# Optimization experiments

Hardware: AMD Instinct MI355X
Metric: run time of the kernel (lower is better)

The kernel has to match this reference:

```python
import jax, jax.numpy as jnp
import numpy as np

H = 4      # num_attention_heads
DK = 75    # d_k = hidden_size // H
HID = 300  # hidden_size


def setup_inputs() -> dict:
    key = jax.random.key(0)
    ks = jax.random.split(key, 9)
    B, S = 8, 2048
    query = jax.random.normal(ks[0], (B, S, HID), dtype=jnp.float32)
    key_t = jax.random.normal(ks[1], (B, S, HID), dtype=jnp.float32)
    value = jax.random.normal(ks[2], (B, S, HID), dtype=jnp.float32)
    mask = jax.random.randint(ks[3], (B, S), 0, 2, dtype=jnp.int32)
    scale = 1.0 / np.sqrt(HID)
    Wq = jax.random.normal(ks[4], (HID, HID), dtype=jnp.float32) * scale
    Wk = jax.random.normal(ks[5], (HID, HID), dtype=jnp.float32) * scale
    Wv = jax.random.normal(ks[6], (HID, HID), dtype=jnp.float32) * scale
    Wo = jax.random.normal(ks[7], (HID, HID), dtype=jnp.float32) * scale
    bo = jax.random.normal(ks[8], (HID,), dtype=jnp.float32) * 0.01
    return {"query": query, "key": key_t, "value": value, "mask": mask,
            "Wq": Wq, "Wk": Wk, "Wv": Wv, "Wo": Wo, "bo": bo}


def reference(query, key, value, mask, Wq, Wk, Wv, Wo, bo):
    B, S, _ = query.shape
    # QKV projections (nn.Linear: x @ W.T), split into heads: [B,H,S,DK]
    def proj(x, W):
        return (x @ W.T).reshape(B, S, H, DK).transpose(0, 2, 1, 3)
    q, k, v = proj(query, Wq), proj(key, Wk), proj(value, Wv)
    # scores: [B,H,S,S]
    scores = jnp.einsum('bhqd,bhkd->bhqk', q, k) / jnp.sqrt(jnp.float32(DK))
    # mask outer product 'bi,bj->bij' broadcast over heads; fill zeros with -1e9
    m2 = (mask[:, :, None] * mask[:, None, :])[:, None, :, :]  # [B,1,S,S]
    scores = jnp.where(m2 == 0, jnp.float32(-1e9), scores)
    p_attn = jax.nn.softmax(scores, axis=-1)  # dropout p=0.0 (eval mode)
    x = jnp.einsum('bhqk,bhkd->bhqd', p_attn, v)  # [B,H,S,DK]
    x = x.transpose(0, 2, 1, 3).reshape(B, S, H * DK)
    return x @ Wo.T + bo
```

## Files before the change

### kernel.cpp

```cpp
#include <hip/hip_runtime.h>
#include <math.h>

typedef __bf16 bf16x8 __attribute__((ext_vector_type(8)));
typedef float f32x4 __attribute__((ext_vector_type(4)));
typedef float f32x16 __attribute__((ext_vector_type(16)));
typedef unsigned short u16;
typedef u16 u16x8 __attribute__((ext_vector_type(8)));

#define HID 300
#define NH 4
#define DK 75
#define DKP 80
#define BB 8
#define SS 2048
#define BSROWS (BB*SS)
#define C2   0.16658807f

#define MFMA(a,b,c)   __builtin_amdgcn_mfma_f32_16x16x32_bf16(a,b,c,0,0,0)
#define MFMA32(a,b,c) __builtin_amdgcn_mfma_f32_32x32x16_bf16(a,b,c,0,0,0)

static __device__ __forceinline__ float bf2f(u16 h) {
    return __uint_as_float(((unsigned)h) << 16);
}
static __device__ __forceinline__ void split2(float x, u16& hb, u16& lb) {
    const unsigned u = __float_as_uint(x);
    hb = (u16)(u >> 16);
    const float r = x - __uint_as_float(u & 0xffff0000u);
    lb = (u16)(__float_as_uint(r) >> 16);
}
static __device__ __forceinline__ void split2rne(float x, u16& hb, u16& lb) {
    const unsigned u = __float_as_uint(x);
    const unsigned uh = ((u + 0x7fffu + ((u >> 16) & 1u)) >> 16) << 16;
    hb = (u16)(uh >> 16);
    const float r = x - __uint_as_float(uh);
    lb = (u16)(__float_as_uint(r) >> 16);
}

__global__ __launch_bounds__(256)
void prep_w3(const float* __restrict__ Wq, const float* __restrict__ Wk,
             const float* __restrict__ Wv,
             u16* __restrict__ wph, u16* __restrict__ wpl)
{
    const int idx = blockIdx.x * 256 + threadIdx.x;
    if (idx >= 38400) return;
    const int c8 = idx % 40;
    int r = idx / 40;
    const int n = r % 80; r /= 80;
    const int h = r & 3;  r >>= 2;
    const int mat = r;
    const float* W = (mat == 0) ? Wq : (mat == 1) ? Wk : Wv;
    const int col0 = c8 * 8;
    float v[8];
#pragma unroll
    for (int j = 0; j < 8; ++j) v[j] = 0.f;
    if (n < DK) {
        const float* s = W + (size_t)(h * DK + n) * HID + col0;
        if (col0 + 8 <= HID) {
#pragma unroll
            for (int j = 0; j < 8; ++j) v[j] = s[j];
        } else {
#pragma unroll
            for (int j = 0; j < 8; ++j) v[j] = (col0 + j < HID) ? s[j] : 0.f;
        }
    }
    u16x8 hv, lv;
#pragma unroll
    for (int j = 0; j < 8; ++j) {
        u16 hb, lb;
        split2(v[j], hb, lb);
        hv[j] = hb; lv[j] = lb;
    }
    const size_t base = ((size_t)((mat * 4 + h) * 80 + n)) * 320 + col0;
    *(u16x8*)(wph + base) = hv;
    *(u16x8*)(wpl + base) = lv;
}

static __device__ __forceinline__ void gemm_body(
    char* smem, const float* __restrict__ A, const float* __restrict__ W,
    const u16* __restrict__ Wph, const u16* __restrict__ Wpl,
    const float* __restrict__ bias, u16* __restrict__ hiP, u16* __restrict__ loP,
    float* __restrict__ foutP, const int mode, const int bx, const int h)
{
    u16* Ah = (u16*)smem;
    u16* Al = Ah + 128 * 40;
    u16* Wh = Al + 128 * 40;
    u16* Wl = Wh + 80 * 40;

    const int t = threadIdx.x;
    const int wv = t >> 6, l = t & 63, qc = l & 15, g = l >> 4;
    const int row0 = bx * 128;
    const int b = row0 >> 11;
    const int s0 = row0 & 2047;

    const f32x4 zf = {0.f, 0.f, 0.f, 0.f};
    f32x4 acc[2][5];
#pragma unroll
    for (int mt = 0; mt < 2; ++mt)
#pragma unroll
        for (int nt = 0; nt < 5; ++nt) acc[mt][nt] = zf;

    const int rA = t >> 1, halfA = t & 1;
    float4 aPf[4];
    u16x8 wPfH[2], wPfL[2];
    float4 wPf2[3];

    auto loadA = [&](int step) {
        const int k0 = step * 32 + halfA * 16;
        const float* src = A + (size_t)(row0 + rA) * HID + k0;
#pragma unroll
        for (int c4 = 0; c4 < 4; ++c4) {
            const int k = k0 + c4 * 4;
            float4 v;
            if (k + 4 <= HID) v = *(const float4*)(src + c4 * 4);
            else {
                v.x = (k + 0 < HID) ? src[c4 * 4 + 0] : 0.f;
                v.y = (k + 1 < HID) ? src[c4 * 4 + 1] : 0.f;
                v.z = (k + 2 < HID) ? src[c4 * 4 + 2] : 0.f;
                v.w = (k + 3 < HID) ? src[c4 * 4 + 3] : 0.f;
            }
            aPf[c4] = v;
        }
    };
    auto loadW = [&](int step) {
        const int k0 = step * 32;
        if (mode <= 1) {
#pragma unroll
            for (int j = 0; j < 2; ++j) {
                const int idx = j * 256 + t;
                if (idx < 320) {
                    const int n = idx >> 2, c = idx & 3;
                    const size_t wo = (size_t)(h * 80 + n) * 320 + k0 + c * 8;
                    wPfH[j] = *(const u16x8*)(Wph + wo);
                    wPfL[j] = *(const u16x8*)(Wpl + wo);
                }
            }
        } else {
#pragma unroll
            for (int j = 0; j < 3; ++j) {
                const int idx = j * 256 + t;
                if (idx < 640) {
                    const int n = idx >> 3, c = idx & 7;
                    const int k = k0 + c * 4;
                    float4 v = make_float4(0.f, 0.f, 0.f, 0.f);
                    if (n < DK) {
                        const float* src = W + (size_t)(h * DK + n) * HID + k;
                        if (k + 4 <= HID) v = *(const float4*)src;
                        else {
                            v.x = (k + 0 < HID) ? src[0] : 0.f;
                            v.y = (k + 1 < HID) ? src[1] : 0.f;
                            v.z = (k + 2 < HID) ? src[2] : 0.f;
                            v.w = (k + 3 < HID) ? src[3] : 0.f;
                        }
                    }
                    wPf2[j] = v;
                }
            }
        }
    };
    auto writeA = [&]() {
        u16* dh = Ah + rA * 40 + halfA * 16;
        u16* dl = Al + rA * 40 + halfA * 16;
#pragma unroll
        for (int c4 = 0; c4 < 4; ++c4) {
            ushort4 h4, l4;
            split2(aPf[c4].x, h4.x, l4.x);
            split2(aPf[c4].y, h4.y, l4.y);
            split2(aPf[c4].z, h4.z, l4.z);
            split2(aPf[c4].w, h4.w, l4.w);
            *(ushort4*)(dh + c4 * 4) = h4;
            *(ushort4*)(dl + c4 * 4) = l4;
        }
    };
    auto writeW = [&]() {
        if (mode <= 1) {
#pragma unroll
            for (int j = 0; j < 2; ++j) {
                const int idx = j * 256 + t;
                if (idx < 320) {
                    const int n = idx >> 2, c = idx & 3;
                    *(u16x8*)(Wh + n * 40 + c * 8) = wPfH[j];
                    *(u16x8*)(Wl + n * 40 + c * 8) = wPfL[j];
                }
            }
        } else {
#pragma unroll
            for (int j = 0; j < 3; ++j) {
                const int idx = j * 256 + t;
                if (idx < 640) {
                    const int n = idx >> 3, c = idx & 7;
                    ushort4 h4, l4;
                    split2(wPf2[j].x, h4.x, l4.x);
                    split2(wPf2[j].y, h4.y, l4.y);
                    split2(wPf2[j].z, h4.z, l4.z);
                    split2(wPf2[j].w, h4.w, l4.w);
                    *(ushort4*)(Wh + n * 40 + c * 4) = h4;
                    *(ushort4*)(Wl + n * 40 + c * 4) = l4;
                }
            }
        }
    };

    loadA(0);
    loadW(0);

    for (int step = 0; step < 10; ++step) {
        __syncthreads();
        writeA();
        writeW();
        __syncthreads();
        if (step < 9) {
            loadA(step + 1);
            loadW(step + 1);
        }
        bf16x8 ah[2], al2[2];
#pragma unroll
        for (int mt = 0; mt < 2; ++mt) {
            const int roff = (wv * 32 + mt * 16 + qc) * 40 + g * 8;
            ah[mt]  = *(const bf16x8*)(Ah + roff);
            al2[mt] = *(const bf16x8*)(Al + roff);
        }
#pragma unroll
        for (int nt = 0; nt < 5; ++nt) {
            const int woff = (nt * 16 + qc) * 40 + g * 8;
            const bf16x8 bh = *(const bf16x8*)(Wh + woff);
            const bf16x8 bl = *(const bf16x8*)(Wl + woff);
#pragma unroll
            for (int mt = 0; mt < 2; ++mt) {
                acc[mt][nt] = MFMA(ah[mt],  bh, acc[mt][nt]);
                acc[mt][nt] = MFMA(al2[mt], bh, acc[mt][nt]);
                acc[mt][nt] = MFMA(ah[mt],  bl, acc[mt][nt]);
            }
        }
    }
    __syncthreads();

    if (mode <= 1) {
        unsigned* epi = (unsigned*)smem;
#pragma unroll
        for (int mt = 0; mt < 2; ++mt)
#pragma unroll
            for (int nt = 0; nt < 5; ++nt)
#pragma unroll
                for (int r = 0; r < 4; ++r) {
                    u16 hb, lb;
                    split2rne(acc[mt][nt][r], hb, lb);
                    epi[(wv * 32 + mt * 16 + g * 4 + r) * 84 + nt * 16 + qc] =
                        (unsigned)hb | ((unsigned)lb << 16);
                }
        __syncthreads();
        if (mode == 0) {
            const int r = t >> 1, half = t & 1;
            const unsigned* row = epi + r * 84 + half * 40;
            const size_t base = ((size_t)(b * NH + h) * SS + s0 + r) * DKP + half * 40;
            u16* dh = hiP + base;
#pragma unroll
            for (int i = 0; i < 5; ++i) {
                u16x8 hv, lv;
#pragma unroll
                for (int j = 0; j < 8; ++j) {
                    const unsigned u = row[i * 8 + j];
                    hv[j] = (u16)u; lv[j] = (u16)(u >> 16);
                }
                *(u16x8*)(dh + i * 8) = hv;
                if (loP) *(u16x8*)(loP + base + i * 8) = lv;
            }
        } else {
#pragma unroll
            for (int i = 0; i < 3; ++i) {
                const int idx = i * 256 + t;
                if (idx < 640) {
                    const int d = idx >> 3, sc = (idx & 7) * 16;
                    const size_t base = ((size_t)(b * NH + h) * DKP + d) * SS + s0 + sc;
                    u16* dh = hiP + base;
                    u16x8 h0, h1, l0, l1;
#pragma unroll
                    for (int j = 0; j < 8; ++j) {
                        unsigned u = epi[(sc + j) * 84 + d];
                        h0[j] = (u16)u; l0[j] = (u16)(u >> 16);
                        u = epi[(sc + 8 + j) * 84 + d];
                        h1[j] = (u16)u; l1[j] = (u16)(u >> 16);
                    }
                    *(u16x8*)dh = h0; *(u16x8*)(dh + 8) = h1;
                    if (loP) {
                        *(u16x8*)(loP + base) = l0;
                        *(u16x8*)(loP + base + 8) = l1;
                    }
                }
            }
        }
    } else {
        float* epf = (float*)smem;
#pragma unroll
        for (int mt = 0; mt < 2; ++mt)
#pragma unroll
            for (int nt = 0; nt < 5; ++nt)
#pragma unroll
                for (int r = 0; r < 4; ++r)
                    epf[(wv * 32 + mt * 16 + g * 4 + r) * 84 + nt * 16 + qc] = acc[mt][nt][r];
        __syncthreads();
        for (int i = 0; i < 38; ++i) {
            const int idx = i * 256 + t;
            if (idx < 128 * DK) {
                const int r = idx / DK, c = idx - r * DK;
                foutP[(size_t)(row0 + r) * HID + h * DK + c] = epf[r * 84 + c] + bias[h * DK + c];
            }
        }
    }
}

__global__ __launch_bounds__(256)
void proj3_gemm(const float* __restrict__ Aq, const float* __restrict__ Ak,
                const float* __restrict__ Av,
                const u16* __restrict__ wph, const u16* __restrict__ wpl,
                u16* __restrict__ qh, u16* __restrict__ ql,
                u16* __restrict__ kh, u16* __restrict__ vh)
{
    __shared__ char smem[43008];
    const int z = blockIdx.z;
    const float* A = (z == 0) ? Aq : (z == 1) ? Ak : Av;
    const size_t WMAT = (size_t)4 * 80 * 320;
    u16* hiP = (z == 0) ? qh : (z == 1) ? kh : vh;
    u16* loP = (z == 0) ? ql : nullptr;
    const int mode = (z == 2) ? 1 : 0;
    gemm_body(smem, A, nullptr, wph + z * WMAT, wpl + z * WMAT,
              nullptr, hiP, loP, nullptr, mode, blockIdx.x, blockIdx.y);
}

__global__ __launch_bounds__(256)
void out_gemm(const float* __restrict__ A, const float* __restrict__ W,
              const float* __restrict__ bias, float* __restrict__ out)
{
    __shared__ char smem[43008];
    gemm_body(smem, A, W, nullptr, nullptr, bias, nullptr, nullptr, out, 2,
              blockIdx.x, blockIdx.y);
}

__global__ __launch_bounds__(256, 2)
void attn_mfma32(const u16* __restrict__ qhi, const u16* __restrict__ qlo,
                 const u16* __restrict__ khi, const u16* __restrict__ vhi,
                 const int* __restrict__ mask, float* __restrict__ xout)
{
    __shared__ u16 KsH[2 * 8192];
    __shared__ u16 VsH[2 * 6144];
    __shared__ u16 Ps[4 * 2048];
    __shared__ int Mw[64];

    const int t = threadIdx.x;
    const int wv = t >> 6;
    const int l = t & 63;
    const int q = l & 31;
    const int hi = l >> 5;

    const int bx = blockIdx.x;
    const int xcd = bx & 7, idx = bx >> 3;
    const int bh = xcd * 4 + (idx & 3);
    const int qt = idx >> 2;
    const int b = bh >> 2;
    const int h = bh & 3;
    const int q0 = qt * 128;

    {
        const int rr = (t >> 4) & 15, o8 = t & 15;
        *(uint2*)(VsH + (80 + rr) * 64 + o8 * 4) = make_uint2(0u, 0u);
        *(uint2*)(VsH + 6144 + (80 + rr) * 64 + o8 * 4) = make_uint2(0u, 0u);
    }
    if (t < 64) {
        const int* mrow = mask + b * SS + t * 32;
        unsigned w = 0;
        for (int j = 0; j < 32; ++j) w |= (mrow[j] != 0 ? 1u : 0u) << j;
        Mw[t] = (int)w;
    }

    const size_t planeQK = (size_t)bh * (SS * DKP);
    const int qrow = q0 + wv * 32 + q;
    const int mq = (mask[b * SS + qrow] != 0);
    const float qscale = mq ? C2 : 0.0f;
    const unsigned wAll = mq ? 0u : 0xffffffffu;

    bf16x8 Qh[5], Ql[5];
    {
        const u16* ph = qhi + planeQK + (size_t)qrow * DKP;
        const u16* pl = qlo + planeQK + (size_t)qrow * DKP;
#pragma unroll
        for (int ch = 0; ch < 5; ++ch) {
            Qh[ch] = *(const bf16x8*)(ph + 16 * ch + 8 * hi);
            Ql[ch] = *(const bf16x8*)(pl + 16 * ch + 8 * hi);
        }
    }

    const u16* kH = khi + planeQK;
    const u16* vH = vhi + (size_t)bh * (DKP * SS);
    u16* PsW = Ps + wv * 2048;

    int kOff[5], kLds[5], vOff[5], vLds[5];
#pragma unroll
    for (int i = 0; i < 5; ++i) {
        const int gi = t + i * 256;
        const int r = gi / 20, c8 = gi % 20;
        kOff[i] = r * 160 + c8 * 8;
        kLds[i] = r * 256 + ((c8 * 8) ^ ((r & 7) << 4));
        const int d = gi >> 4, cv = gi & 15;
        vOff[i] = d * 4096 + cv * 8;
        vLds[i] = d * 128 + ((cv * 8) ^ ((d & 7) << 4));
    }

    uint2 kr[5], vr[5];
#define LOADT(KT) do { _Pragma("unroll") \
    for (int i = 0; i < 5; ++i) { \
        kr[i] = *(const uint2*)((const char*)kH + (size_t)(KT) * 10240 + kOff[i]); \
        vr[i] = *(const uint2*)((const char*)vH + (size_t)(KT) * 128 + vOff[i]); \
    } } while (0)
#define WRITET(BUF) do { _Pragma("unroll") \
    for (int i = 0; i < 5; ++i) { \
        *(uint2*)((char*)(KsH + (BUF) * 8192) + kLds[i]) = kr[i]; \
        *(uint2*)((char*)(VsH + (BUF) * 6144) + vLds[i]) = vr[i]; \
    } } while (0)

    LOADT(0);
    WRITET(0);
    LOADT(1);
    __syncthreads();

    f32x16 O[3];
#pragma unroll
    for (int dt = 0; dt < 3; ++dt) O[dt] = (f32x16){};
    float ll = 0.f;
    const int kswz = (q & 7) << 4;
    const int pswz = kswz;

    for (int kt = 0; kt < 32; ++kt) {
        const int cur = kt & 1;
        const char* Kc = (const char*)(KsH + cur * 8192);
        const char* Vc = (const char*)(VsH + cur * 6144);

        f32x16 s0 = (f32x16){}, s1 = (f32x16){};
#pragma unroll
        for (int ch = 0; ch < 5; ++ch) {
            const int o = (32 * ch + 16 * hi) ^ kswz;
            const bf16x8 a0 = *(const bf16x8*)(Kc + q * 256 + o);
            const bf16x8 a1 = *(const bf16x8*)(Kc + (32 + q) * 256 + o);
            s0 = MFMA32(a0, Qh[ch], s0);
            s0 = MFMA32(a0, Ql[ch], s0);
            s1 = MFMA32(a1, Qh[ch], s1);
            s1 = MFMA32(a1, Ql[ch], s1);
        }

        const unsigned wsel0 = ((unsigned)Mw[2 * kt]) | wAll;
        const unsigned wsel1 = ((unsigned)Mw[2 * kt + 1]) | wAll;
        float ts = 0.f;
        u16 pb0[16], pb1[16];
#pragma unroll
        for (int r = 0; r < 16; ++r) {
            const int srow = (r & 3) + 8 * (r >> 2) + 4 * hi;
            const float e0 = exp2f(s0[r] * qscale);
            const float e1 = exp2f(s1[r] * qscale);
            const u16 t0 = (u16)(__float_as_uint(e0) >> 16);
            const u16 t1 = (u16)(__float_as_uint(e1) >> 16);
            pb0[r] = ((wsel0 >> srow) & 1u) ? t0 : (u16)0;
            pb1[r] = ((wsel1 >> srow) & 1u) ? t1 : (u16)0;
            ts += bf2f(pb0[r]) + bf2f(pb1[r]);
        }
        ts += __shfl_xor(ts, 32);
        ll += ts;

#pragma unroll
        for (int rr = 0; rr < 4; ++rr) {
            ushort4 w4a, w4b;
            w4a.x = pb0[4 * rr + 0]; w4a.y = pb0[4 * rr + 1];
            w4a.z = pb0[4 * rr + 2]; w4a.w = pb0[4 * rr + 3];
            w4b.x = pb1[4 * rr + 0]; w4b.y = pb1[4 * rr + 1];
            w4b.z = pb1[4 * rr + 2]; w4b.w = pb1[4 * rr + 3];
            const int o0 = (16 * rr + 8 * hi) ^ pswz;
            const int o1 = (64 + 16 * rr + 8 * hi) ^ pswz;
            *(ushort4*)((char*)PsW + q * 128 + o0) = w4a;
            *(ushort4*)((char*)PsW + q * 128 + o1) = w4b;
        }

#pragma unroll
        for (int c = 0; c < 4; ++c) {
            const int po = q * 128 + ((32 * c + 16 * hi) ^ pswz);
            const bf16x8 pA = *(const bf16x8*)((char*)PsW + po);
#pragma unroll
            for (int dt = 0; dt < 3; ++dt) {
                const int drow = 32 * dt + q;
                const int vb = drow * 128 + ((32 * c + 16 * hi) ^ ((drow & 7) << 4));
                const bf16x8 vh8 = *(const bf16x8*)(Vc + vb);
                O[dt] = MFMA32(vh8, pA, O[dt]);
            }
        }

        if (kt < 31) {
            WRITET(cur ^ 1);
            if (kt < 30) LOADT(kt + 2);
        }
        __syncthreads();
    }
#undef LOADT
#undef WRITET

    {
        const float inv = 1.0f / ll;
        float* o = xout + (size_t)(b * SS + qrow) * HID + h * DK;
#pragma unroll
        for (int dt = 0; dt < 3; ++dt)
#pragma unroll
            for (int r = 0; r < 16; ++r) {
                const int d = 32 * dt + (r & 3) + 8 * (r >> 2) + 4 * hi;
                if (d < DK) o[d] = O[dt][r] * inv;
            }
    }
}

extern "C" void kernel_launch(void* const* d_in, const int* in_sizes, int n_in,
                              void* d_out, int out_size, void* d_ws, size_t ws_size,
                              hipStream_t stream)
{
    const float* query = (const float*)d_in[0];
    const float* key_t = (const float*)d_in[1];
    const float* value = (const float*)d_in[2];
    const int*   mask  = (const int*)d_in[3];
    const float* Wq    = (const float*)d_in[4];
    const float* Wk    = (const float*)d_in[5];
    const float* Wv    = (const float*)d_in[6];
    const float* Wo    = (const float*)d_in[7];
    const float* bo    = (const float*)d_in[8];
    float* out = (float*)d_out;

    const size_t PL = (size_t)BB * NH * SS * DKP;
    u16* qh = (u16*)d_ws;
    u16* ql = qh + PL;
    u16* kh = ql + PL;
    u16* kl = kh + PL;   (void)kl;
    u16* vh = kl + PL;
    u16* vl = vh + PL;
    float* xws = (float*)(vl + PL);
    u16* wph = (u16*)xws;
    u16* wpl = wph + (size_t)3 * 4 * 80 * 320;

    const dim3 blk(256, 1, 1);

    prep_w3<<<150, blk, 0, stream>>>(Wq, Wk, Wv, wph, wpl);

    proj3_gemm<<<dim3(128, NH, 3), blk, 0, stream>>>(query, key_t, value,
                                                     wph, wpl,
                                                     qh, ql, kh, vh);

    attn_mfma32<<<dim3(512, 1, 1), blk, 0, stream>>>(qh, ql, kh, vh, mask, xws);

    out_gemm<<<dim3(128, NH, 1), blk, 0, stream>>>(xws, Wo, bo, out);
}
```

Before: 194.5 us.

## Fold mask and scale into padded QK columns and keep P in registers

The softmax scale is folded into Q during projection. The key mask is encoded as a bias column in the padded head dimension (Q gets 1.0, K gets 0 or a large negative value), so the mask is applied inside the QK MFMA. Query-side masking is done by zeroing Q. P is no longer staged through LDS: it is packed to bf16 with hardware conversion and rearranged across lanes with v_permlane32_swap, which removes the Ps buffer and the bitmask setup. Smaller V LDS plus launch bounds of 3 aim for higher occupancy. The changes alter rounding (RNE bf16 for P, a bias instead of a select for the mask) and rely on exp2 underflowing for masked keys.

```diff
diff --git a/kernel.cpp b/kernel.cpp
--- a/kernel.cpp
+++ b/kernel.cpp
@@ -19,9 +19,6 @@
 #define MFMA(a,b,c)   __builtin_amdgcn_mfma_f32_16x16x32_bf16(a,b,c,0,0,0)
 #define MFMA32(a,b,c) __builtin_amdgcn_mfma_f32_32x32x16_bf16(a,b,c,0,0,0)
 
-static __device__ __forceinline__ float bf2f(u16 h) {
-    return __uint_as_float(((unsigned)h) << 16);
-}
 static __device__ __forceinline__ void split2(float x, u16& hb, u16& lb) {
     const unsigned u = __float_as_uint(x);
     hb = (u16)(u >> 16);
@@ -34,6 +31,14 @@
     hb = (u16)(uh >> 16);
     const float r = x - __uint_as_float(uh);
     lb = (u16)(__float_as_uint(r) >> 16);
+}
+static __device__ __forceinline__ unsigned pkbf(float a, float b) {
+    const unsigned short ua = __builtin_bit_cast(unsigned short, (__bf16)a);
+    const unsigned short ub = __builtin_bit_cast(unsigned short, (__bf16)b);
+    return (unsigned)ua | ((unsigned)ub << 16);
+}
+static __device__ __forceinline__ void swap32(unsigned& x, unsigned& y) {
+    asm("v_permlane32_swap_b32 %0, %1" : "+v"(x), "+v"(y));
 }
 
 __global__ __launch_bounds__(256)
@@ -79,7 +84,8 @@
     char* smem, const float* __restrict__ A, const float* __restrict__ W,
     const u16* __restrict__ Wph, const u16* __restrict__ Wpl,
     const float* __restrict__ bias, u16* __restrict__ hiP, u16* __restrict__ loP,
-    float* __restrict__ foutP, const int mode, const int bx, const int h)
+    float* __restrict__ foutP, const int mode, const int bx, const int h,
+    const int* __restrict__ pmask, const float scale, const int patch)
 {
     u16* Ah = (u16*)smem;
     u16* Al = Ah + 128 * 40;
@@ -243,7 +249,15 @@
 #pragma unroll
                 for (int r = 0; r < 4; ++r) {
                     u16 hb, lb;
-                    split2rne(acc[mt][nt][r], hb, lb);
+                    split2rne(acc[mt][nt][r] * scale, hb, lb);
+                    if (patch != 0 && nt == 4 && qc == 11) {
+                        if (patch == 1) { hb = (u16)0x3F80; lb = 0; }
+                        else {
+                            const int sr = s0 + wv * 32 + mt * 16 + g * 4 + r;
+                            hb = (pmask[b * SS + sr] != 0) ? (u16)0 : (u16)0xC320;
+                            lb = 0;
+                        }
+                    }
                     epi[(wv * 32 + mt * 16 + g * 4 + r) * 84 + nt * 16 + qc] =
                         (unsigned)hb | ((unsigned)lb << 16);
                 }
@@ -310,7 +324,7 @@
 
 __global__ __launch_bounds__(256)
 void proj3_gemm(const float* __restrict__ Aq, const float* __restrict__ Ak,
-                const float* __restrict__ Av,
+                const float* __restrict__ Av, const int* __restrict__ mask,
                 const u16* __restrict__ wph, const u16* __restrict__ wpl,
                 u16* __restrict__ qh, u16* __restrict__ ql,
                 u16* __restrict__ kh, u16* __restrict__ vh)
@@ -322,8 +336,11 @@
     u16* hiP = (z == 0) ? qh : (z == 1) ? kh : vh;
     u16* loP = (z == 0) ? ql : nullptr;
     const int mode = (z == 2) ? 1 : 0;
+    const float scale = (z == 0) ? C2 : 1.0f;
+    const int patch = (z == 0) ? 1 : (z == 1) ? 2 : 0;
     gemm_body(smem, A, nullptr, wph + z * WMAT, wpl + z * WMAT,
-              nullptr, hiP, loP, nullptr, mode, blockIdx.x, blockIdx.y);
+              nullptr, hiP, loP, nullptr, mode, blockIdx.x, blockIdx.y,
+              mask, scale, patch);
 }
 
 __global__ __launch_bounds__(256)
@@ -332,18 +349,17 @@
 {
     __shared__ char smem[43008];
     gemm_body(smem, A, W, nullptr, nullptr, bias, nullptr, nullptr, out, 2,
-              blockIdx.x, blockIdx.y);
-}
-
-__global__ __launch_bounds__(256, 2)
+              blockIdx.x, blockIdx.y, nullptr, 1.0f, 0);
+}
+
+__global__ __launch_bounds__(256, 3)
 void attn_mfma32(const u16* __restrict__ qhi, const u16* __restrict__ qlo,
                  const u16* __restrict__ khi, const u16* __restrict__ vhi,
                  const int* __restrict__ mask, float* __restrict__ xout)
 {
     __shared__ u16 KsH[2 * 8192];
-    __shared__ u16 VsH[2 * 6144];
-    __shared__ u16 Ps[4 * 2048];
-    __shared__ int Mw[64];
+    __shared__ u16 VsH[2 * 5120];
+    __shared__ u16 VsZ[64];
 
     const int t = threadIdx.x;
     const int wv = t >> 6;
@@ -359,23 +375,12 @@
     const int h = bh & 3;
     const int q0 = qt * 128;
 
-    {
-        const int rr = (t >> 4) & 15, o8 = t & 15;
-        *(uint2*)(VsH + (80 + rr) * 64 + o8 * 4) = make_uint2(0u, 0u);
-        *(uint2*)(VsH + 6144 + (80 + rr) * 64 + o8 * 4) = make_uint2(0u, 0u);
-    }
-    if (t < 64) {
-        const int* mrow = mask + b * SS + t * 32;
-        unsigned w = 0;
-        for (int j = 0; j < 32; ++j) w |= (mrow[j] != 0 ? 1u : 0u) << j;
-        Mw[t] = (int)w;
-    }
+    if (t < 16) *(uint2*)(VsZ + t * 4) = make_uint2(0u, 0u);
 
     const size_t planeQK = (size_t)bh * (SS * DKP);
     const int qrow = q0 + wv * 32 + q;
     const int mq = (mask[b * SS + qrow] != 0);
-    const float qscale = mq ? C2 : 0.0f;
-    const unsigned wAll = mq ? 0u : 0xffffffffu;
+    const u16x8 qm = (u16x8)(u16)(mq ? 0xFFFFu : 0u);
 
     bf16x8 Qh[5], Ql[5];
     {
@@ -383,14 +388,15 @@
         const u16* pl = qlo + planeQK + (size_t)qrow * DKP;
 #pragma unroll
         for (int ch = 0; ch < 5; ++ch) {
-            Qh[ch] = *(const bf16x8*)(ph + 16 * ch + 8 * hi);
-            Ql[ch] = *(const bf16x8*)(pl + 16 * ch + 8 * hi);
+            u16x8 ua = *(const u16x8*)(ph + 16 * ch + 8 * hi) & qm;
+            u16x8 ub = *(const u16x8*)(pl + 16 * ch + 8 * hi) & qm;
+            Qh[ch] = *(bf16x8*)&ua;
+            Ql[ch] = *(bf16x8*)&ub;
         }
     }
 
     const u16* kH = khi + planeQK;
     const u16* vH = vhi + (size_t)bh * (DKP * SS);
-    u16* PsW = Ps + wv * 2048;
 
     int kOff[5], kLds[5], vOff[5], vLds[5];
 #pragma unroll
@@ -412,8 +418,8 @@
     } } while (0)
 #define WRITET(BUF) do { _Pragma("unroll") \
     for (int i = 0; i < 5; ++i) { \
-        *(uint2*)((char*)(KsH + (BUF) * 8192) + kLds[i]) = kr[i]; \
-        *(uint2*)((char*)(VsH + (BUF) * 6144) + vLds[i]) = vr[i]; \
+        *(uint2*)((char*)KsH + (BUF) * 16384 + kLds[i]) = kr[i]; \
+        *(uint2*)((char*)VsH + (BUF) * 10240 + vLds[i]) = vr[i]; \
     } } while (0)
 
     LOADT(0);
@@ -426,12 +432,15 @@
     for (int dt = 0; dt < 3; ++dt) O[dt] = (f32x16){};
     float ll = 0.f;
     const int kswz = (q & 7) << 4;
-    const int pswz = kswz;
+    const int drow2 = 64 + q;
+    const int vsw2 = (drow2 & 7) << 4;
+    const int voff2 = drow2 * 128;
+    const bool z2 = (drow2 >= 80);
 
     for (int kt = 0; kt < 32; ++kt) {
         const int cur = kt & 1;
-        const char* Kc = (const char*)(KsH + cur * 8192);
-        const char* Vc = (const char*)(VsH + cur * 6144);
+        const char* Kc = (const char*)KsH + cur * 16384;
+        const char* Vc = (const char*)VsH + cur * 10240;
 
         f32x16 s0 = (f32x16){}, s1 = (f32x16){};
 #pragma unroll
@@ -445,47 +454,47 @@
             s1 = MFMA32(a1, Ql[ch], s1);
         }
 
-        const unsigned wsel0 = ((unsigned)Mw[2 * kt]) | wAll;
-        const unsigned wsel1 = ((unsigned)Mw[2 * kt + 1]) | wAll;
-        float ts = 0.f;
-        u16 pb0[16], pb1[16];
-#pragma unroll
-        for (int r = 0; r < 16; ++r) {
-            const int srow = (r & 3) + 8 * (r >> 2) + 4 * hi;
-            const float e0 = exp2f(s0[r] * qscale);
-            const float e1 = exp2f(s1[r] * qscale);
-            const u16 t0 = (u16)(__float_as_uint(e0) >> 16);
-            const u16 t1 = (u16)(__float_as_uint(e1) >> 16);
-            pb0[r] = ((wsel0 >> srow) & 1u) ? t0 : (u16)0;
-            pb1[r] = ((wsel1 >> srow) & 1u) ? t1 : (u16)0;
-            ts += bf2f(pb0[r]) + bf2f(pb1[r]);
-        }
-        ts += __shfl_xor(ts, 32);
-        ll += ts;
-
-#pragma unroll
-        for (int rr = 0; rr < 4; ++rr) {
-            ushort4 w4a, w4b;
-            w4a.x = pb0[4 * rr + 0]; w4a.y = pb0[4 * rr + 1];
-            w4a.z = pb0[4 * rr + 2]; w4a.w = pb0[4 * rr + 3];
-            w4b.x = pb1[4 * rr + 0]; w4b.y = pb1[4 * rr + 1];
-            w4b.z = pb1[4 * rr + 2]; w4b.w = pb1[4 * rr + 3];
-            const int o0 = (16 * rr + 8 * hi) ^ pswz;
-            const int o1 = (64 + 16 * rr + 8 * hi) ^ pswz;
-            *(ushort4*)((char*)PsW + q * 128 + o0) = w4a;
-            *(ushort4*)((char*)PsW + q * 128 + o1) = w4b;
-        }
+        float p0 = 0.f, p1 = 0.f, p2 = 0.f, p3 = 0.f;
+        bf16x8 pA[4];
+#pragma unroll
+        for (int sb = 0; sb < 2; ++sb) {
+            const f32x16 sv = sb ? s1 : s0;
+            float e[16];
+#pragma unroll
+            for (int r = 0; r < 16; r += 4) {
+                e[r + 0] = __builtin_amdgcn_exp2f(sv[r + 0]);
+                e[r + 1] = __builtin_amdgcn_exp2f(sv[r + 1]);
+                e[r + 2] = __builtin_amdgcn_exp2f(sv[r + 2]);
+                e[r + 3] = __builtin_amdgcn_exp2f(sv[r + 3]);
+                p0 += e[r + 0]; p1 += e[r + 1]; p2 += e[r + 2]; p3 += e[r + 3];
+            }
+#pragma unroll
+            for (int hf = 0; hf < 2; ++hf) {
+                unsigned X1 = pkbf(e[hf * 8 + 0], e[hf * 8 + 1]);
+                unsigned Y1 = pkbf(e[hf * 8 + 4], e[hf * 8 + 5]);
+                unsigned X2 = pkbf(e[hf * 8 + 2], e[hf * 8 + 3]);
+                unsigned Y2 = pkbf(e[hf * 8 + 6], e[hf * 8 + 7]);
+                swap32(X1, Y1);
+                swap32(X2, Y2);
+                union { unsigned u[4]; bf16x8 v; } cv_;
+                cv_.u[0] = X1; cv_.u[1] = X2; cv_.u[2] = Y1; cv_.u[3] = Y2;
+                pA[sb * 2 + hf] = cv_.v;
+            }
+        }
+        ll += (p0 + p1) + (p2 + p3);
 
 #pragma unroll
         for (int c = 0; c < 4; ++c) {
-            const int po = q * 128 + ((32 * c + 16 * hi) ^ pswz);
-            const bf16x8 pA = *(const bf16x8*)((char*)PsW + po);
-#pragma unroll
-            for (int dt = 0; dt < 3; ++dt) {
-                const int drow = 32 * dt + q;
-                const int vb = drow * 128 + ((32 * c + 16 * hi) ^ ((drow & 7) << 4));
+#pragma unroll
+            for (int dt = 0; dt < 2; ++dt) {
+                const int vb = (32 * dt + q) * 128 + ((32 * c + 16 * hi) ^ kswz);
                 const bf16x8 vh8 = *(const bf16x8*)(Vc + vb);
-                O[dt] = MFMA32(vh8, pA, O[dt]);
+                O[dt] = MFMA32(vh8, pA[c], O[dt]);
+            }
+            {
+                const char* b2 = z2 ? (const char*)VsZ : (Vc + voff2);
+                const bf16x8 vh8 = *(const bf16x8*)(b2 + ((32 * c + 16 * hi) ^ vsw2));
+                O[2] = MFMA32(vh8, pA[c], O[2]);
             }
         }
 
@@ -498,6 +507,7 @@
 #undef LOADT
 #undef WRITET
 
+    ll += __shfl_xor(ll, 32);
     {
         const float inv = 1.0f / ll;
         float* o = xout + (size_t)(b * SS + qrow) * HID + h * DK;
@@ -541,7 +551,7 @@
 
     prep_w3<<<150, blk, 0, stream>>>(Wq, Wk, Wv, wph, wpl);
 
-    proj3_gemm<<<dim3(128, NH, 3), blk, 0, stream>>>(query, key_t, value,
+    proj3_gemm<<<dim3(128, NH, 3), blk, 0, stream>>>(query, key_t, value, mask,
                                                      wph, wpl,
                                                      qh, ql, kh, vh);
 
```

Measured after the change: 221.3 us. 1.14x slower.
